# Optimization experiments

Hardware: AMD Instinct MI355X
Metric: run time of the kernel (lower is better)

Reference implementation:

```python
import jax, jax.numpy as jnp
import numpy as np
import math

B, T, C = 4, 2048, 1024
N_HEAD = 16


def setup_inputs() -> dict:
    key = jax.random.key(0)
    k1, k2, k3 = jax.random.split(key, 3)
    x = jax.random.normal(k1, (B, T, C), dtype=jnp.float32)
    W_attn = jax.random.normal(k2, (C, 3 * C), dtype=jnp.float32) * (1.0 / math.sqrt(C))
    b_attn = jnp.zeros((3 * C,), dtype=jnp.float32)
    W_proj = jax.random.normal(k3, (C, C), dtype=jnp.float32) * (1.0 / math.sqrt(C))
    b_proj = jnp.zeros((C,), dtype=jnp.float32)
    return {"x": x, "W_attn": W_attn, "b_attn": b_attn, "W_proj": W_proj, "b_proj": b_proj}


def reference(x, W_attn, b_attn, W_proj, b_proj):
    b, t, c = x.shape
    hs = c // N_HEAD  # head size
    qkv = x @ W_attn + b_attn  # [B,T,3C]
    q, k, v = jnp.split(qkv, 3, axis=-1)
    # [B,T,C] -> [B,H,T,hs]
    q = q.reshape(b, t, N_HEAD, hs).transpose(0, 2, 1, 3)
    k = k.reshape(b, t, N_HEAD, hs).transpose(0, 2, 1, 3)
    v = v.reshape(b, t, N_HEAD, hs).transpose(0, 2, 1, 3)
    att = jnp.einsum('bhqd,bhkd->bhqk', q, k) / math.sqrt(hs)  # [B,H,T,T]
    causal = jnp.tril(jnp.ones((t, t), dtype=bool))
    att = jnp.where(causal[None, None, :, :], att, -jnp.inf)
    att = jax.nn.softmax(att, axis=-1)
    y = jnp.einsum('bhqk,bhkd->bhqd', att, v)  # [B,H,T,hs]
    y = y.transpose(0, 2, 1, 3).reshape(b, t, c)
    return y @ W_proj + b_proj
```

## Files before the change

kernel.cpp:

```cpp
#include <hip/hip_runtime.h>


typedef __bf16 bf16_t;
typedef __bf16 bf16x8 __attribute__((ext_vector_type(8)));
typedef __bf16 bf16x4 __attribute__((ext_vector_type(4)));
typedef float  f32x4  __attribute__((ext_vector_type(4)));

#define MFMA16(a, b, c) __builtin_amdgcn_mfma_f32_16x16x32_bf16((a), (b), (c), 0, 0, 0)

static __device__ __forceinline__ void gld_lds16(const bf16_t* g, void* l) {
  __builtin_amdgcn_global_load_lds(
      (const __attribute__((address_space(1))) void*)(const void*)g,
      (__attribute__((address_space(3))) void*)l, 16, 0, 0);
}

static __device__ __forceinline__ bf16x8 ldv8(const void* p) {
  return *reinterpret_cast<const bf16x8*>(p);
}

static __device__ __forceinline__ float exp2_hw(float x) {
  float r;
  asm("v_exp_f32 %0, %1" : "=v"(r) : "v"(x));
  return r;
}

__global__ __launch_bounds__(256) void cvt_f32_bf16(const float* __restrict__ in,
                                                    bf16_t* __restrict__ out, int n4) {
  int i = blockIdx.x * 256 + threadIdx.x;
  if (i < n4) {
    float4 v = reinterpret_cast<const float4*>(in)[i];
    bf16x4 o;
    o[0] = (bf16_t)v.x; o[1] = (bf16_t)v.y; o[2] = (bf16_t)v.z; o[3] = (bf16_t)v.w;
    reinterpret_cast<bf16x4*>(out)[i] = o;
  }
}

__global__ __launch_bounds__(256) void transpose_cvt(const float* __restrict__ in,
                                                     bf16_t* __restrict__ out,
                                                     int Kd, int Nd) {
  __shared__ float tile[32][33];
  int tx = threadIdx.x, ty = threadIdx.y;
  int n0 = blockIdx.x * 32, k0 = blockIdx.y * 32;
#pragma unroll
  for (int i = 0; i < 4; ++i)
    tile[ty + i * 8][tx] = in[(size_t)(k0 + ty + i * 8) * Nd + (n0 + tx)];
  __syncthreads();
#pragma unroll
  for (int i = 0; i < 4; ++i)
    out[(size_t)(n0 + ty + i * 8) * Kd + (k0 + tx)] = (bf16_t)tile[tx][ty + i * 8];
}

template <int MODE>
__global__ __launch_bounds__(512) void gemm8p(
    const bf16_t* __restrict__ A, const bf16_t* __restrict__ Bt,
    const float* __restrict__ bias, int M, int N, int K,
    bf16_t* __restrict__ Qo, bf16_t* __restrict__ Ko, bf16_t* __restrict__ Vt,
    float* __restrict__ Co) {
  __shared__ alignas(16) char lds[147456];

  const int tid = threadIdx.x;
  const int wave = tid >> 6, lane = tid & 63;
  const int wm = wave >> 2, wn = wave & 3;
  const int l16 = lane & 15, kb = lane >> 4;
  const int r7 = l16 & 7;

  const int nbx = gridDim.x;
  const int lb = blockIdx.y * nbx + blockIdx.x;
  const int c = lb & 7;
  const int ii = lb >> 3;
  const int rPer = gridDim.y >> 3;
  const int tmt = c * rPer + (ii % rPer);
  const int tnt = ii / rPer;
  const int tm0 = tmt * 256, tn0 = tnt * 128;

  const int srow = tid >> 3;
  const int sch = (tid & 7) ^ (srow & 7);
  const bf16_t* aR = A + (size_t)(tm0 + srow) * K + sch * 8;
  const bf16_t* bR = Bt + (size_t)(tn0 + srow) * K + sch * 8;

  auto stageA = [&](int buf, int kt) {
    char* d = lds + buf * 49152 + wave * 1024;
    const bf16_t* s = aR + kt * 64;
#pragma unroll
    for (int i = 0; i < 4; ++i)
      gld_lds16(s + (size_t)(i * 64) * K, d + i * 8192);
  };
  auto stageB = [&](int buf, int kt) {
    char* d = lds + buf * 49152 + 32768 + wave * 1024;
    const bf16_t* s = bR + kt * 64;
#pragma unroll
    for (int i = 0; i < 2; ++i)
      gld_lds16(s + (size_t)(i * 64) * K, d + i * 8192);
  };

  f32x4 acc[8][2] = {};
  const int NK = K >> 6;

  stageA(0, 0); stageB(0, 0);
  stageA(1, 1); stageB(1, 1);
  asm volatile("s_waitcnt vmcnt(6)" ::: "memory");
  __builtin_amdgcn_s_barrier();
  __builtin_amdgcn_sched_barrier(0);

  for (int kt = 0; kt < NK; ++kt) {
    const int buf = kt % 3;
    const char* Ab = lds + buf * 49152;
    const char* Bb = Ab + 32768;
    const int nkt = kt + 2;
    const int arow = wm * 128 + l16;
    const int brow = wn * 32 + l16;

    {
      bf16x8 af[8], bfr[2];
#pragma unroll
      for (int m = 0; m < 8; ++m)
        af[m] = ldv8(Ab + (arow + m * 16) * 128 + ((kb ^ r7) * 16));
#pragma unroll
      for (int nq = 0; nq < 2; ++nq)
        bfr[nq] = ldv8(Bb + (brow + nq * 16) * 128 + ((kb ^ r7) * 16));
      if (nkt < NK) stageA(nkt % 3, nkt);
      __builtin_amdgcn_s_barrier();
      asm volatile("s_waitcnt lgkmcnt(0)" ::: "memory");
      __builtin_amdgcn_sched_barrier(0);
      __builtin_amdgcn_s_setprio(1);
#pragma unroll
      for (int m = 0; m < 8; ++m) {
        acc[m][0] = MFMA16(af[m], bfr[0], acc[m][0]);
        acc[m][1] = MFMA16(af[m], bfr[1], acc[m][1]);
      }
      __builtin_amdgcn_s_setprio(0);
      __builtin_amdgcn_s_barrier();
      __builtin_amdgcn_sched_barrier(0);
    }

    {
      bf16x8 af[8], bfr[2];
#pragma unroll
      for (int m = 0; m < 8; ++m)
        af[m] = ldv8(Ab + (arow + m * 16) * 128 + (((4 + kb) ^ r7) * 16));
#pragma unroll
      for (int nq = 0; nq < 2; ++nq)
        bfr[nq] = ldv8(Bb + (brow + nq * 16) * 128 + (((4 + kb) ^ r7) * 16));
      if (nkt < NK) stageB(nkt % 3, nkt);
      __builtin_amdgcn_s_barrier();
      asm volatile("s_waitcnt lgkmcnt(0)" ::: "memory");
      __builtin_amdgcn_sched_barrier(0);
      __builtin_amdgcn_s_setprio(1);
#pragma unroll
      for (int m = 0; m < 8; ++m) {
        acc[m][0] = MFMA16(af[m], bfr[0], acc[m][0]);
        acc[m][1] = MFMA16(af[m], bfr[1], acc[m][1]);
      }
      __builtin_amdgcn_s_setprio(0);
      if (kt + 1 < NK) {
        if (nkt < NK) {
          asm volatile("s_waitcnt vmcnt(6)" ::: "memory");
        } else {
          asm volatile("s_waitcnt vmcnt(0)" ::: "memory");
        }
      }
      __builtin_amdgcn_s_barrier();
      __builtin_amdgcn_sched_barrier(0);
    }
  }

#pragma unroll
  for (int nq = 0; nq < 2; ++nq) {
    const int n = tn0 + wn * 32 + nq * 16 + l16;
    const float bv = bias[n];
#pragma unroll
    for (int mi = 0; mi < 8; ++mi) {
#pragma unroll
      for (int j = 0; j < 4; ++j) {
        const int m = tm0 + wm * 128 + mi * 16 + kb * 4 + j;
        const float v = acc[mi][nq][j] + bv;
        if constexpr (MODE == 0) {
          const int which = n >> 10, hn = n & 1023;
          const int h = hn >> 6, d = hn & 63;
          const int b = m >> 11, t = m & 2047;
          const size_t bh = (size_t)(b * 16 + h);
          if (which == 0)
            Qo[(bh * 2048 + t) * 64 + d] = (bf16_t)(v * 0.18033688011112042f);
          else if (which == 1)
            Ko[(bh * 2048 + t) * 64 + d] = (bf16_t)v;
          else
            Vt[(bh * 64 + d) * 2048 + t] = (bf16_t)v;
        } else {
          Co[(size_t)m * N + n] = v;
        }
      }
    }
  }
}

__global__ __launch_bounds__(256) void attn_fwd(const bf16_t* __restrict__ Qg,
                                                const bf16_t* __restrict__ Kg,
                                                const bf16_t* __restrict__ Vtg,
                                                bf16_t* __restrict__ Yg) {
  __shared__ alignas(16) char lds[40960];

  const int tid = threadIdx.x;
  const int wave = tid >> 6, lane = tid & 63;
  const int l16 = lane & 15, kb = lane >> 4;
  const int l8 = l16 & 7;
  const float NEG_INF = -__builtin_inff();

  const int n = blockIdx.x;
  const int bh = (n & 7) * 8 + ((n >> 3) & 7);
  const int qt = 31 - (n >> 6);
  const size_t base = (size_t)bh * (2048 * 64);
  const int b = bh >> 4, h = bh & 15;

  const int srow = tid >> 3;
  const int schunk = (tid & 7) ^ (srow & 7);
  const bf16_t* Ksrc = Kg + base + (size_t)srow * 64 + schunk * 8;
  const bf16_t* Vsrc = Vtg + base + (size_t)srow * 2048 + schunk * 8;

  auto stageK = [&](int buf, int kv0) {
    char* kd = lds + buf * 8192 + wave * 1024;
    const bf16_t* ks = Ksrc + (size_t)kv0 * 64;
    gld_lds16(ks, kd);
    gld_lds16(ks + 2048, kd + 4096);
  };
  auto stageV = [&](int buf, int kv0) {
    char* vd = lds + 16384 + buf * 8192 + wave * 1024;
    const bf16_t* vs = Vsrc + kv0;
    gld_lds16(vs, vd);
    gld_lds16(vs + 65536, vd + 4096);
  };

  const int q0 = qt * 64 + wave * 16;
  const int q = q0 + l16;
  const int trips = qt + 1;

  const bf16x8 qf0 = ldv8(Qg + base + (size_t)q * 64 + kb * 8);
  const bf16x8 qf1 = ldv8(Qg + base + (size_t)q * 64 + 32 + kb * 8);

  f32x4 o[4] = {};
  float m_r = NEG_INF, l_r = 0.f;

  char* Pw = lds + 32768 + wave * 2048;

  stageK(0, 0);
  stageV(0, 0);
  asm volatile("s_waitcnt vmcnt(0)" ::: "memory");
  __builtin_amdgcn_s_barrier();
  __builtin_amdgcn_sched_barrier(0);

  int cur = 0;
  for (int t = 0; t < trips; ++t) {
    const int kv0 = t * 64;
    const bool more = (t + 1 < trips);
    if (more) {
      stageK(cur ^ 1, kv0 + 64);
      stageV(cur ^ 1, kv0 + 64);
    }

    const char* Kb = lds + cur * 8192;
    const char* Vb = lds + 16384 + cur * 8192;

    bf16x8 kf[8];
#pragma unroll
    for (int i = 0; i < 4; ++i) {
      const int row = i * 16 + l16;
#pragma unroll
      for (int kc = 0; kc < 2; ++kc)
        kf[i * 2 + kc] = ldv8(Kb + row * 128 + (((kc * 4 + kb) ^ (row & 7)) * 16));
    }

    f32x4 s[4] = {};
    __builtin_amdgcn_s_setprio(1);
#pragma unroll
    for (int i = 0; i < 4; ++i) {
      s[i] = MFMA16(kf[i * 2 + 0], qf0, s[i]);
      s[i] = MFMA16(kf[i * 2 + 1], qf1, s[i]);
    }
    __builtin_amdgcn_s_setprio(0);

    bf16x8 vf[8];
#pragma unroll
    for (int i = 0; i < 4; ++i) {
      const int row = i * 16 + l16;
#pragma unroll
      for (int kc = 0; kc < 2; ++kc)
        vf[i * 2 + kc] = ldv8(Vb + row * 128 + (((kc * 4 + kb) ^ (row & 7)) * 16));
    }

    float pm[4];
    if (t == qt) {
#pragma unroll
      for (int i = 0; i < 4; ++i) {
        f32x4 sv = s[i];
#pragma unroll
        for (int j = 0; j < 4; ++j)
          if (kv0 + i * 16 + kb * 4 + j > q) sv[j] = NEG_INF;
        s[i] = sv;
        pm[i] = fmaxf(fmaxf(sv[0], sv[1]), fmaxf(sv[2], sv[3]));
      }
    } else {
#pragma unroll
      for (int i = 0; i < 4; ++i)
        pm[i] = fmaxf(fmaxf(s[i][0], s[i][1]), fmaxf(s[i][2], s[i][3]));
    }
    float mx = fmaxf(fmaxf(pm[0], pm[1]), fmaxf(pm[2], pm[3]));
    if (__any(mx > m_r + 8.0f)) {
      mx = fmaxf(mx, __shfl_xor(mx, 16));
      mx = fmaxf(mx, __shfl_xor(mx, 32));
      const float mn = fmaxf(m_r, mx);
      const float sc = exp2_hw(m_r - mn);
      l_r *= sc;
#pragma unroll
      for (int i = 0; i < 4; ++i) {
        o[i][0] *= sc; o[i][1] *= sc; o[i][2] *= sc; o[i][3] *= sc;
      }
      m_r = mn;
    }
    float ss = 0.f;
    bf16x4 pw[4];
#pragma unroll
    for (int i = 0; i < 4; ++i)
#pragma unroll
      for (int j = 0; j < 4; ++j) {
        const float p = exp2_hw(s[i][j] - m_r);
        ss += p;
        pw[i][j] = (bf16_t)p;
      }
    l_r += ss;

#pragma unroll
    for (int i = 0; i < 4; ++i) {
      const int phys = (i * 2 + (kb >> 1)) ^ l8;
      *reinterpret_cast<bf16x4*>(Pw + l16 * 128 + phys * 16 + (kb & 1) * 8) = pw[i];
    }
    const bf16x8 pb0 = ldv8(Pw + l16 * 128 + ((kb ^ l8) * 16));
    const bf16x8 pb1 = ldv8(Pw + l16 * 128 + (((4 + kb) ^ l8) * 16));

    __builtin_amdgcn_s_setprio(1);
#pragma unroll
    for (int i = 0; i < 4; ++i) {
      o[i] = MFMA16(vf[i * 2 + 0], pb0, o[i]);
      o[i] = MFMA16(vf[i * 2 + 1], pb1, o[i]);
    }
    __builtin_amdgcn_s_setprio(0);

    asm volatile("s_waitcnt vmcnt(0)" ::: "memory");
    __builtin_amdgcn_s_barrier();
    __builtin_amdgcn_sched_barrier(0);
    cur ^= 1;
  }

  float lt = l_r + __shfl_xor(l_r, 16);
  lt += __shfl_xor(lt, 32);
  const float inv = 1.0f / lt;
  bf16_t* yrow = Yg + ((size_t)(b * 2048 + q)) * 1024 + h * 64;
#pragma unroll
  for (int i = 0; i < 4; ++i) {
    bf16x4 yv;
    yv[0] = (bf16_t)(o[i][0] * inv);
    yv[1] = (bf16_t)(o[i][1] * inv);
    yv[2] = (bf16_t)(o[i][2] * inv);
    yv[3] = (bf16_t)(o[i][3] * inv);
    *reinterpret_cast<bf16x4*>(yrow + i * 16 + kb * 4) = yv;
  }
}

extern "C" void kernel_launch(void* const* d_in, const int* in_sizes, int n_in,
                              void* d_out, int out_size, void* d_ws, size_t ws_size,
                              hipStream_t stream) {
  const float* x = (const float*)d_in[0];
  const float* W_attn = (const float*)d_in[1];
  const float* b_attn = (const float*)d_in[2];
  const float* W_proj = (const float*)d_in[3];
  const float* b_proj = (const float*)d_in[4];
  float* out = (float*)d_out;

  char* ws = (char*)d_ws;
  bf16_t* xb  = (bf16_t*)(ws + 0);
  bf16_t* WaT = (bf16_t*)(ws + 16777216);
  bf16_t* WpT = (bf16_t*)(ws + 23068672);
  bf16_t* Qb  = (bf16_t*)(ws + 25165824);
  bf16_t* Kb  = (bf16_t*)(ws + 41943040);
  bf16_t* Vt  = (bf16_t*)(ws + 58720256);
  bf16_t* Yb  = (bf16_t*)(ws + 75497472);

  cvt_f32_bf16<<<8192, 256, 0, stream>>>(x, xb, 8192 * 1024 / 4);
  transpose_cvt<<<dim3(96, 32), dim3(32, 8), 0, stream>>>(W_attn, WaT, 1024, 3072);
  transpose_cvt<<<dim3(32, 32), dim3(32, 8), 0, stream>>>(W_proj, WpT, 1024, 1024);

  gemm8p<0><<<dim3(24, 32), 512, 0, stream>>>(xb, WaT, b_attn, 8192, 3072, 1024,
                                              Qb, Kb, Vt, nullptr);

  attn_fwd<<<2048, 256, 0, stream>>>(Qb, Kb, Vt, Yb);

  gemm8p<1><<<dim3(8, 32), 512, 0, stream>>>(Yb, WpT, b_proj, 8192, 1024, 1024,
                                             nullptr, nullptr, nullptr, out);
}
```

Measured before the change: 185.8 us.

## Enlarge GEMM tiles to 256x256 with double-buffered LDS staging

Changes both GEMMs from 256x128 to 256x256 output tiles per 512-thread block. Each wave now computes a 128x64 sub-tile (acc[8][4]), which improves operand reuse from LDS and halves global reloads of A. The LDS pipeline drops from triple to double buffering, and each iteration is split into four MFMA quadrant phases that overlap the next A and B stages. The cost is fewer blocks (384 and 128) on a machine with many CUs, a shallower prefetch, higher register pressure, and a full vmcnt(0) wait on every iteration.

```diff
diff --git a/kernel.cpp b/kernel.cpp
--- a/kernel.cpp
+++ b/kernel.cpp
@@ -51,12 +51,12 @@
 }
 
 template <int MODE>
-__global__ __launch_bounds__(512) void gemm8p(
+__global__ __launch_bounds__(512) void gemm256(
     const bf16_t* __restrict__ A, const bf16_t* __restrict__ Bt,
     const float* __restrict__ bias, int M, int N, int K,
     bf16_t* __restrict__ Qo, bf16_t* __restrict__ Ko, bf16_t* __restrict__ Vt,
     float* __restrict__ Co) {
-  __shared__ alignas(16) char lds[147456];
+  __shared__ alignas(16) char lds[131072];
 
   const int tid = threadIdx.x;
   const int wave = tid >> 6, lane = tid & 63;
@@ -71,7 +71,7 @@
   const int rPer = gridDim.y >> 3;
   const int tmt = c * rPer + (ii % rPer);
   const int tnt = ii / rPer;
-  const int tm0 = tmt * 256, tn0 = tnt * 128;
+  const int tm0 = tmt * 256, tn0 = tnt * 256;
 
   const int srow = tid >> 3;
   const int sch = (tid & 7) ^ (srow & 7);
@@ -79,101 +79,126 @@
   const bf16_t* bR = Bt + (size_t)(tn0 + srow) * K + sch * 8;
 
   auto stageA = [&](int buf, int kt) {
-    char* d = lds + buf * 49152 + wave * 1024;
+    char* d = lds + buf * 65536 + wave * 1024;
     const bf16_t* s = aR + kt * 64;
 #pragma unroll
     for (int i = 0; i < 4; ++i)
       gld_lds16(s + (size_t)(i * 64) * K, d + i * 8192);
   };
   auto stageB = [&](int buf, int kt) {
-    char* d = lds + buf * 49152 + 32768 + wave * 1024;
+    char* d = lds + buf * 65536 + 32768 + wave * 1024;
     const bf16_t* s = bR + kt * 64;
 #pragma unroll
-    for (int i = 0; i < 2; ++i)
+    for (int i = 0; i < 4; ++i)
       gld_lds16(s + (size_t)(i * 64) * K, d + i * 8192);
   };
 
-  f32x4 acc[8][2] = {};
+  f32x4 acc[8][4] = {};
   const int NK = K >> 6;
 
   stageA(0, 0); stageB(0, 0);
-  stageA(1, 1); stageB(1, 1);
-  asm volatile("s_waitcnt vmcnt(6)" ::: "memory");
+  asm volatile("s_waitcnt vmcnt(0)" ::: "memory");
   __builtin_amdgcn_s_barrier();
   __builtin_amdgcn_sched_barrier(0);
 
   for (int kt = 0; kt < NK; ++kt) {
-    const int buf = kt % 3;
-    const char* Ab = lds + buf * 49152;
+    const int buf = kt & 1;
+    const char* Ab = lds + buf * 65536;
     const char* Bb = Ab + 32768;
-    const int nkt = kt + 2;
+    const bool more = (kt + 1 < NK);
     const int arow = wm * 128 + l16;
-    const int brow = wn * 32 + l16;
-
-    {
-      bf16x8 af[8], bfr[2];
-#pragma unroll
-      for (int m = 0; m < 8; ++m)
-        af[m] = ldv8(Ab + (arow + m * 16) * 128 + ((kb ^ r7) * 16));
-#pragma unroll
-      for (int nq = 0; nq < 2; ++nq)
-        bfr[nq] = ldv8(Bb + (brow + nq * 16) * 128 + ((kb ^ r7) * 16));
-      if (nkt < NK) stageA(nkt % 3, nkt);
-      __builtin_amdgcn_s_barrier();
-      asm volatile("s_waitcnt lgkmcnt(0)" ::: "memory");
-      __builtin_amdgcn_sched_barrier(0);
-      __builtin_amdgcn_s_setprio(1);
-#pragma unroll
-      for (int m = 0; m < 8; ++m) {
-        acc[m][0] = MFMA16(af[m], bfr[0], acc[m][0]);
-        acc[m][1] = MFMA16(af[m], bfr[1], acc[m][1]);
-      }
-      __builtin_amdgcn_s_setprio(0);
-      __builtin_amdgcn_s_barrier();
-      __builtin_amdgcn_sched_barrier(0);
-    }
-
-    {
-      bf16x8 af[8], bfr[2];
-#pragma unroll
-      for (int m = 0; m < 8; ++m)
-        af[m] = ldv8(Ab + (arow + m * 16) * 128 + (((4 + kb) ^ r7) * 16));
-#pragma unroll
-      for (int nq = 0; nq < 2; ++nq)
-        bfr[nq] = ldv8(Bb + (brow + nq * 16) * 128 + (((4 + kb) ^ r7) * 16));
-      if (nkt < NK) stageB(nkt % 3, nkt);
-      __builtin_amdgcn_s_barrier();
-      asm volatile("s_waitcnt lgkmcnt(0)" ::: "memory");
-      __builtin_amdgcn_sched_barrier(0);
-      __builtin_amdgcn_s_setprio(1);
-#pragma unroll
-      for (int m = 0; m < 8; ++m) {
-        acc[m][0] = MFMA16(af[m], bfr[0], acc[m][0]);
-        acc[m][1] = MFMA16(af[m], bfr[1], acc[m][1]);
-      }
-      __builtin_amdgcn_s_setprio(0);
-      if (kt + 1 < NK) {
-        if (nkt < NK) {
-          asm volatile("s_waitcnt vmcnt(6)" ::: "memory");
-        } else {
-          asm volatile("s_waitcnt vmcnt(0)" ::: "memory");
-        }
-      }
-      __builtin_amdgcn_s_barrier();
-      __builtin_amdgcn_sched_barrier(0);
-    }
+    const int brow = wn * 64 + l16;
+
+    bf16x8 af[4][2], b0[2][2], b1[2][2];
+
+#pragma unroll
+    for (int mi = 0; mi < 4; ++mi)
+#pragma unroll
+      for (int kc = 0; kc < 2; ++kc)
+        af[mi][kc] = ldv8(Ab + (arow + mi * 16) * 128 + (((kc * 4 + kb) ^ r7) * 16));
+#pragma unroll
+    for (int ni = 0; ni < 2; ++ni)
+#pragma unroll
+      for (int kc = 0; kc < 2; ++kc)
+        b0[ni][kc] = ldv8(Bb + (brow + ni * 16) * 128 + (((kc * 4 + kb) ^ r7) * 16));
+    if (more) stageA(buf ^ 1, kt + 1);
+    __builtin_amdgcn_s_barrier();
+    asm volatile("s_waitcnt lgkmcnt(0)" ::: "memory");
+    __builtin_amdgcn_sched_barrier(0);
+    __builtin_amdgcn_s_setprio(1);
+#pragma unroll
+    for (int mi = 0; mi < 4; ++mi)
+#pragma unroll
+      for (int ni = 0; ni < 2; ++ni)
+#pragma unroll
+        for (int kc = 0; kc < 2; ++kc)
+          acc[mi][ni] = MFMA16(af[mi][kc], b0[ni][kc], acc[mi][ni]);
+    __builtin_amdgcn_s_setprio(0);
+    __builtin_amdgcn_s_barrier();
+
+#pragma unroll
+    for (int ni = 0; ni < 2; ++ni)
+#pragma unroll
+      for (int kc = 0; kc < 2; ++kc)
+        b1[ni][kc] = ldv8(Bb + (brow + (2 + ni) * 16) * 128 + (((kc * 4 + kb) ^ r7) * 16));
+    if (more) stageB(buf ^ 1, kt + 1);
+    __builtin_amdgcn_s_barrier();
+    asm volatile("s_waitcnt lgkmcnt(0)" ::: "memory");
+    __builtin_amdgcn_sched_barrier(0);
+    __builtin_amdgcn_s_setprio(1);
+#pragma unroll
+    for (int mi = 0; mi < 4; ++mi)
+#pragma unroll
+      for (int ni = 0; ni < 2; ++ni)
+#pragma unroll
+        for (int kc = 0; kc < 2; ++kc)
+          acc[mi][2 + ni] = MFMA16(af[mi][kc], b1[ni][kc], acc[mi][2 + ni]);
+    __builtin_amdgcn_s_setprio(0);
+    __builtin_amdgcn_s_barrier();
+
+#pragma unroll
+    for (int mi = 0; mi < 4; ++mi)
+#pragma unroll
+      for (int kc = 0; kc < 2; ++kc)
+        af[mi][kc] = ldv8(Ab + (arow + (4 + mi) * 16) * 128 + (((kc * 4 + kb) ^ r7) * 16));
+    __builtin_amdgcn_s_barrier();
+    asm volatile("s_waitcnt lgkmcnt(0)" ::: "memory");
+    __builtin_amdgcn_sched_barrier(0);
+    __builtin_amdgcn_s_setprio(1);
+#pragma unroll
+    for (int mi = 0; mi < 4; ++mi)
+#pragma unroll
+      for (int ni = 0; ni < 2; ++ni)
+#pragma unroll
+        for (int kc = 0; kc < 2; ++kc)
+          acc[4 + mi][ni] = MFMA16(af[mi][kc], b0[ni][kc], acc[4 + mi][ni]);
+    __builtin_amdgcn_s_setprio(0);
+    __builtin_amdgcn_s_barrier();
+
+    __builtin_amdgcn_s_setprio(1);
+#pragma unroll
+    for (int mi = 0; mi < 4; ++mi)
+#pragma unroll
+      for (int ni = 0; ni < 2; ++ni)
+#pragma unroll
+        for (int kc = 0; kc < 2; ++kc)
+          acc[4 + mi][2 + ni] = MFMA16(af[mi][kc], b1[ni][kc], acc[4 + mi][2 + ni]);
+    __builtin_amdgcn_s_setprio(0);
+    if (more) asm volatile("s_waitcnt vmcnt(0)" ::: "memory");
+    __builtin_amdgcn_s_barrier();
+    __builtin_amdgcn_sched_barrier(0);
   }
 
 #pragma unroll
-  for (int nq = 0; nq < 2; ++nq) {
-    const int n = tn0 + wn * 32 + nq * 16 + l16;
+  for (int ni = 0; ni < 4; ++ni) {
+    const int n = tn0 + wn * 64 + ni * 16 + l16;
     const float bv = bias[n];
 #pragma unroll
     for (int mi = 0; mi < 8; ++mi) {
 #pragma unroll
       for (int j = 0; j < 4; ++j) {
         const int m = tm0 + wm * 128 + mi * 16 + kb * 4 + j;
-        const float v = acc[mi][nq][j] + bv;
+        const float v = acc[mi][ni][j] + bv;
         if constexpr (MODE == 0) {
           const int which = n >> 10, hn = n & 1023;
           const int h = hn >> 6, d = hn & 63;
@@ -387,11 +412,11 @@
   transpose_cvt<<<dim3(96, 32), dim3(32, 8), 0, stream>>>(W_attn, WaT, 1024, 3072);
   transpose_cvt<<<dim3(32, 32), dim3(32, 8), 0, stream>>>(W_proj, WpT, 1024, 1024);
 
-  gemm8p<0><<<dim3(24, 32), 512, 0, stream>>>(xb, WaT, b_attn, 8192, 3072, 1024,
-                                              Qb, Kb, Vt, nullptr);
+  gemm256<0><<<dim3(12, 32), 512, 0, stream>>>(xb, WaT, b_attn, 8192, 3072, 1024,
+                                               Qb, Kb, Vt, nullptr);
 
   attn_fwd<<<2048, 256, 0, stream>>>(Qb, Kb, Vt, Yb);
 
-  gemm8p<1><<<dim3(8, 32), 512, 0, stream>>>(Yb, WpT, b_proj, 8192, 1024, 1024,
-                                             nullptr, nullptr, nullptr, out);
-}
+  gemm256<1><<<dim3(4, 32), 512, 0, stream>>>(Yb, WpT, b_proj, 8192, 1024, 1024,
+                                              nullptr, nullptr, nullptr, out);
+}
```

Measured after the change: 209.6 us. +12.8%, slower.
